# Kernel optimization log

Measured on AMD Instinct MI355X. Metric: run time of the kernel, lower is better.

## Reference

```python
import jax, jax.numpy as jnp
import numpy as np

EPS = 1e-6
KH, KW = 3, 3
SH, SW = 1, 1


def _unfold(x, kh, kw, sh, sw):
    # x: [N, C, H, W] -> patches [N, C, kh*kw, L], L = ox*oy (torch.nn.Unfold layout)
    N, C, H, W = x.shape
    ox = (H - kh) // sh + 1
    oy = (W - kw) // sw + 1
    pats = [x[:, :, i:i + sh * ox:sh, j:j + sw * oy:sw]
            for i in range(kh) for j in range(kw)]
    p = jnp.stack(pats, axis=2)  # [N, C, K, ox, oy]
    return p.reshape(N, C, kh * kw, ox * oy), ox, oy


def setup_inputs() -> dict:
    key = jax.random.key(0)
    kx, k1, k2 = jax.random.split(key, 3)
    x = jax.random.uniform(kx, (32, 2, 64, 64, 64), dtype=jnp.float32)
    w1 = jax.random.uniform(k1, (64, KH * KW), dtype=jnp.float32)
    w2 = jax.random.uniform(k2, (128, 64), dtype=jnp.float32)
    return {"x": x, "w1": w1, "w2": w2}


def reference(x, w1, w2):
    B = x.shape[0]
    out_ch = w2.shape[0]
    xr = x[:, 0]  # rotation plane [B, C, H, W]
    xa = x[:, 1]  # magnitude plane

    pr, ox, oy = _unfold(xr, KH, KW, SH, SW)  # [B, C, K, L]
    pa, _, _ = _unfold(xa, KH, KW, SH, SW)

    # weightNormalize1: squared weights normalized by GLOBAL sum (rot branch)
    w1_glob = w1 ** 2 / jnp.sum(w1 ** 2)
    w2_glob = w2 ** 2 / jnp.sum(w2 ** 2)
    # weightNormalize (drop_prob=0): squared weights normalized PER ROW (abs branch)
    w1_row = w1 ** 2 / jnp.sum(w1 ** 2, axis=1, keepdims=True)
    w2_row = w2 ** 2 / jnp.sum(w2 ** 2, axis=1, keepdims=True)

    # rotation branch: two weighted contractions
    rot = jnp.einsum('bckl,ck->bcl', pr, w1_glob)          # [B, C, L]
    out_rot = jnp.einsum('bcl,oc->bol', rot, w2_glob)      # [B, O, L]
    out_rot = out_rot.reshape(B, 1, out_ch, ox, oy)

    # magnitude branch: log -> weighted contractions -> exp
    la = jnp.log(pa + EPS)                                  # [B, C, K, L]
    a1 = jnp.einsum('bckl,ck->bcl', la, w1_row)             # [B, C, L]
    out_abs = jnp.exp(jnp.einsum('bcl,oc->bol', a1, w2_row))
    out_abs = out_abs.reshape(B, 1, out_ch, ox, oy)

    return jnp.concatenate([out_rot, out_abs], axis=1)  # [B, 2, O, ox, oy]
```

## Files before the change

### kernel.cpp

```cpp
#include <hip/hip_runtime.h>
#include <cstdint>
#include <cstddef>

#define EPSF 1e-6f

typedef __attribute__((ext_vector_type(4))) float f32x4;
typedef __attribute__((ext_vector_type(8))) short s16x8;

static __device__ __forceinline__ unsigned short f2bf(float f) {
    unsigned u = __float_as_uint(f);
    u += 0x7FFFu + ((u >> 16) & 1u);
    return (unsigned short)(u >> 16);
}
static __device__ __forceinline__ float bf2f(unsigned short h) {
    return __uint_as_float(((unsigned)h) << 16);
}
static __device__ __forceinline__ unsigned packHL(float v) {
    unsigned short h = f2bf(v);
    float r = v - bf2f(h);
    unsigned short l = f2bf(r);
    return ((unsigned)h << 16) | (unsigned)l;
}

__global__ __launch_bounds__(256) void prep_weights(const float* __restrict__ w1,
                                                    const float* __restrict__ w2,
                                                    float* __restrict__ ws) {
    __shared__ float part1[4], part2[4];
    __shared__ float s1row[64];
    __shared__ float s2row[128];
    __shared__ float tot[2];

    const int t = threadIdx.x;
    const int ln = t & 63;
    const int wv = t >> 6;

    float s1 = 0.f;
    for (int i = t; i < 64 * 9; i += 256) { float v = w1[i]; s1 += v * v; }
    float s2 = 0.f;
    const float4* w2v = (const float4*)w2;
    for (int i = t; i < 2048; i += 256) {
        float4 v = w2v[i];
        s2 += v.x * v.x + v.y * v.y + v.z * v.z + v.w * v.w;
    }
    #pragma unroll
    for (int d = 32; d > 0; d >>= 1) {
        s1 += __shfl_down(s1, d);
        s2 += __shfl_down(s2, d);
    }
    if (ln == 0) { part1[wv] = s1; part2[wv] = s2; }

    if (t < 64) {
        float rs = 0.f;
        #pragma unroll
        for (int k = 0; k < 9; ++k) { float v = w1[t * 9 + k]; rs += v * v; }
        s1row[t] = rs;
    } else if (t < 192) {
        const int o = t - 64;
        float rs = 0.f;
        const float4* p = (const float4*)(w2 + o * 64);
        #pragma unroll
        for (int k = 0; k < 16; ++k) {
            float4 v = p[k];
            rs += v.x * v.x + v.y * v.y + v.z * v.z + v.w * v.w;
        }
        s2row[o] = rs;
    }
    __syncthreads();
    if (t == 0) tot[0] = part1[0] + part1[1] + part1[2] + part1[3];
    if (t == 1) tot[1] = part2[0] + part2[1] + part2[2] + part2[3];
    __syncthreads();

    const float t1 = tot[0];
    const float t2 = tot[1];
    for (int i = t; i < 64 * 9; i += 256) {
        float q = w1[i] * w1[i];
        ws[i] = q / t1;
        ws[576 + i] = q / s1row[i / 9];
    }
    unsigned* wsu = (unsigned*)ws;
    for (int i = t; i < 8192; i += 256) {
        float q = w2[i] * w2[i];
        wsu[1152 + i]        = packHL(q / t2);
        wsu[1152 + 8192 + i] = packHL(q / s2row[i >> 6]);
    }
}

__global__ __launch_bounds__(256) void conv_fused(const float* __restrict__ x,
                                                  const float* __restrict__ ws,
                                                  float* __restrict__ out) {
    const int h = blockIdx.x;
    const int branch = blockIdx.y;
    const int b = blockIdx.z;
    const int t = threadIdx.x;
    const int lane = t & 63;
    const int wv = __builtin_amdgcn_readfirstlane(t >> 6);
    const int lm = lane & 15;
    const int quad = lane >> 4;

    __shared__ unsigned rotT[64 * 65];

    const float* __restrict__ w1n = ws + branch * 576;
    const unsigned* __restrict__ w2p = (const unsigned*)ws + 1152 + branch * 8192;
    const float* __restrict__ xb = x + (size_t)(b * 2 + branch) * (64 * 4096);

    #pragma unroll 4
    for (int i = 0; i < 16; ++i) {
        const int c = wv * 16 + i;
        const float* xp = xb + c * 4096 + h * 64 + lane;
        float r0 = xp[0];
        float r1 = xp[64];
        float r2 = xp[128];
        if (branch) {
            r0 = __logf(r0 + EPSF);
            r1 = __logf(r1 + EPSF);
            r2 = __logf(r2 + EPSF);
        }
        const float* wc = w1n + c * 9;
        const float a1 = __shfl_down(r0, 1), a2 = __shfl_down(r0, 2);
        const float b1 = __shfl_down(r1, 1), b2 = __shfl_down(r1, 2);
        const float c1 = __shfl_down(r2, 1), c2 = __shfl_down(r2, 2);
        float s = r0 * wc[0] + a1 * wc[1] + a2 * wc[2]
                + r1 * wc[3] + b1 * wc[4] + b2 * wc[5]
                + r2 * wc[6] + c1 * wc[7] + c2 * wc[8];
        rotT[lane * 65 + c] = packHL(s);
    }
    __syncthreads();

    s16x8 aH[2][2], aL[2][2];
    #pragma unroll
    for (int mt = 0; mt < 2; ++mt) {
        #pragma unroll
        for (int kk = 0; kk < 2; ++kk) {
            const unsigned* p = w2p + (wv * 32 + mt * 16 + lm) * 64 + kk * 32 + quad * 8;
            #pragma unroll
            for (int j = 0; j < 8; ++j) {
                unsigned u = p[j];
                aH[mt][kk][j] = (short)(u >> 16);
                aL[mt][kk][j] = (short)(u & 0xffffu);
            }
        }
    }

    f32x4 acc[2][4];
    #pragma unroll
    for (int mt = 0; mt < 2; ++mt)
        #pragma unroll
        for (int nt = 0; nt < 4; ++nt)
            acc[mt][nt] = (f32x4){0.f, 0.f, 0.f, 0.f};

    #pragma unroll
    for (int nt = 0; nt < 4; ++nt) {
        #pragma unroll
        for (int kk = 0; kk < 2; ++kk) {
            const unsigned* lp = &rotT[(nt * 16 + lm) * 65 + kk * 32 + quad * 8];
            s16x8 bH, bL;
            #pragma unroll
            for (int j = 0; j < 8; ++j) {
                unsigned u = lp[j];
                bH[j] = (short)(u >> 16);
                bL[j] = (short)(u & 0xffffu);
            }
            #pragma unroll
            for (int mt = 0; mt < 2; ++mt) {
                acc[mt][nt] = __builtin_amdgcn_mfma_f32_16x16x32_bf16(aH[mt][kk], bH, acc[mt][nt], 0, 0, 0);
                acc[mt][nt] = __builtin_amdgcn_mfma_f32_16x16x32_bf16(aH[mt][kk], bL, acc[mt][nt], 0, 0, 0);
                acc[mt][nt] = __builtin_amdgcn_mfma_f32_16x16x32_bf16(aL[mt][kk], bH, acc[mt][nt], 0, 0, 0);
            }
        }
    }

    #pragma unroll
    for (int mt = 0; mt < 2; ++mt) {
        const int oc0 = wv * 32 + mt * 16 + quad * 4;
        #pragma unroll
        for (int nt = 0; nt < 4; ++nt) {
            const int px = nt * 16 + lm;
            if (px < 62) {
                const size_t base =
                    ((size_t)((b * 2 + branch) * 128 + oc0)) * 3844 + (size_t)h * 62 + px;
                #pragma unroll
                for (int r = 0; r < 4; ++r) {
                    float v = acc[mt][nt][r];
                    if (branch) v = __expf(v);
                    out[base + (size_t)r * 3844] = v;
                }
            }
        }
    }
}

extern "C" void kernel_launch(void* const* d_in, const int* in_sizes, int n_in,
                              void* d_out, int out_size, void* d_ws, size_t ws_size,
                              hipStream_t stream) {
    const float* x  = (const float*)d_in[0];
    const float* w1 = (const float*)d_in[1];
    const float* w2 = (const float*)d_in[2];
    float* out = (float*)d_out;
    float* ws  = (float*)d_ws;

    prep_weights<<<1, 256, 0, stream>>>(w1, w2, ws);

    dim3 grid(62, 2, 32);
    conv_fused<<<grid, 256, 0, stream>>>(x, ws, out);
}
```

Measured before the change: 238.6 us.

## Vectorize depthwise stage with float4 loads and perm-based bf16 split

Result: faster. 219.1 us (-8.1%).

```diff
diff --git a/kernel.cpp b/kernel.cpp
--- a/kernel.cpp
+++ b/kernel.cpp
@@ -6,6 +6,7 @@
 
 typedef __attribute__((ext_vector_type(4))) float f32x4;
 typedef __attribute__((ext_vector_type(8))) short s16x8;
+typedef union { s16x8 v; unsigned u[4]; } s16x8u;
 
 static __device__ __forceinline__ unsigned short f2bf(float f) {
     unsigned u = __float_as_uint(f);
@@ -73,9 +74,12 @@
     const float t1 = tot[0];
     const float t2 = tot[1];
     for (int i = t; i < 64 * 9; i += 256) {
+        const int c = i / 9;
+        const int k = i - c * 9;
+        const int idx = (c >> 4) * 144 + (c & 3) * 36 + ((c >> 2) & 3) * 9 + k;
         float q = w1[i] * w1[i];
-        ws[i] = q / t1;
-        ws[576 + i] = q / s1row[i / 9];
+        ws[idx] = q / t1;
+        ws[576 + idx] = q / s1row[c];
     }
     unsigned* wsu = (unsigned*)ws;
     for (int i = t; i < 8192; i += 256) {
@@ -96,50 +100,80 @@
     const int wv = __builtin_amdgcn_readfirstlane(t >> 6);
     const int lm = lane & 15;
     const int quad = lane >> 4;
+    const int c4 = lm;
+    const int chsub = quad;
 
     __shared__ unsigned rotT[64 * 65];
 
-    const float* __restrict__ w1n = ws + branch * 576;
+    const float* __restrict__ w1t = ws + branch * 576;
     const unsigned* __restrict__ w2p = (const unsigned*)ws + 1152 + branch * 8192;
     const float* __restrict__ xb = x + (size_t)(b * 2 + branch) * (64 * 4096);
 
-    #pragma unroll 4
-    for (int i = 0; i < 16; ++i) {
-        const int c = wv * 16 + i;
-        const float* xp = xb + c * 4096 + h * 64 + lane;
-        float r0 = xp[0];
-        float r1 = xp[64];
-        float r2 = xp[128];
+    const float* xrow = xb + h * 64 + 4 * c4;
+    #pragma unroll 2
+    for (int cg = 0; cg < 4; ++cg) {
+        const int c = wv * 16 + cg * 4 + chsub;
+        const float* xp = xrow + c * 4096;
+        float4 v0 = *(const float4*)xp;
+        float4 v1 = *(const float4*)(xp + 64);
+        float4 v2 = *(const float4*)(xp + 128);
         if (branch) {
-            r0 = __logf(r0 + EPSF);
-            r1 = __logf(r1 + EPSF);
-            r2 = __logf(r2 + EPSF);
-        }
-        const float* wc = w1n + c * 9;
-        const float a1 = __shfl_down(r0, 1), a2 = __shfl_down(r0, 2);
-        const float b1 = __shfl_down(r1, 1), b2 = __shfl_down(r1, 2);
-        const float c1 = __shfl_down(r2, 1), c2 = __shfl_down(r2, 2);
-        float s = r0 * wc[0] + a1 * wc[1] + a2 * wc[2]
-                + r1 * wc[3] + b1 * wc[4] + b2 * wc[5]
-                + r2 * wc[6] + c1 * wc[7] + c2 * wc[8];
-        rotT[lane * 65 + c] = packHL(s);
-    }
-    __syncthreads();
-
-    s16x8 aH[2][2], aL[2][2];
+            v0.x = __logf(v0.x + EPSF); v0.y = __logf(v0.y + EPSF);
+            v0.z = __logf(v0.z + EPSF); v0.w = __logf(v0.w + EPSF);
+            v1.x = __logf(v1.x + EPSF); v1.y = __logf(v1.y + EPSF);
+            v1.z = __logf(v1.z + EPSF); v1.w = __logf(v1.w + EPSF);
+            v2.x = __logf(v2.x + EPSF); v2.y = __logf(v2.y + EPSF);
+            v2.z = __logf(v2.z + EPSF); v2.w = __logf(v2.w + EPSF);
+        }
+        const float sx0 = __shfl_down(v0.x, 1), sy0 = __shfl_down(v0.y, 1);
+        const float sx1 = __shfl_down(v1.x, 1), sy1 = __shfl_down(v1.y, 1);
+        const float sx2 = __shfl_down(v2.x, 1), sy2 = __shfl_down(v2.y, 1);
+        const float* wc = w1t + wv * 144 + chsub * 36 + cg * 9;
+        const float w0 = wc[0], w1_ = wc[1], w2_ = wc[2];
+        const float w3 = wc[3], w4 = wc[4], w5 = wc[5];
+        const float w6 = wc[6], w7 = wc[7], w8 = wc[8];
+        float p0 = v0.x * w0 + v0.y * w1_ + v0.z * w2_
+                 + v1.x * w3 + v1.y * w4  + v1.z * w5
+                 + v2.x * w6 + v2.y * w7  + v2.z * w8;
+        float p1 = v0.y * w0 + v0.z * w1_ + v0.w * w2_
+                 + v1.y * w3 + v1.z * w4  + v1.w * w5
+                 + v2.y * w6 + v2.z * w7  + v2.w * w8;
+        float p2 = v0.z * w0 + v0.w * w1_ + sx0 * w2_
+                 + v1.z * w3 + v1.w * w4  + sx1 * w5
+                 + v2.z * w6 + v2.w * w7  + sx2 * w8;
+        float p3 = v0.w * w0 + sx0 * w1_ + sy0 * w2_
+                 + v1.w * w3 + sx1 * w4  + sy1 * w5
+                 + v2.w * w6 + sx2 * w7  + sy2 * w8;
+        unsigned* rp = &rotT[(4 * c4) * 65 + c];
+        rp[0]   = packHL(p0);
+        rp[65]  = packHL(p1);
+        rp[130] = packHL(p2);
+        rp[195] = packHL(p3);
+    }
+
+    unsigned araw[2][2][8];
     #pragma unroll
     for (int mt = 0; mt < 2; ++mt) {
         #pragma unroll
         for (int kk = 0; kk < 2; ++kk) {
             const unsigned* p = w2p + (wv * 32 + mt * 16 + lm) * 64 + kk * 32 + quad * 8;
             #pragma unroll
-            for (int j = 0; j < 8; ++j) {
-                unsigned u = p[j];
-                aH[mt][kk][j] = (short)(u >> 16);
-                aL[mt][kk][j] = (short)(u & 0xffffu);
-            }
-        }
-    }
+            for (int j = 0; j < 8; ++j) araw[mt][kk][j] = p[j];
+        }
+    }
+    __syncthreads();
+
+    s16x8u aH[2][2], aL[2][2];
+    #pragma unroll
+    for (int mt = 0; mt < 2; ++mt)
+        #pragma unroll
+        for (int kk = 0; kk < 2; ++kk)
+            #pragma unroll
+            for (int j2 = 0; j2 < 4; ++j2) {
+                unsigned u0 = araw[mt][kk][2 * j2], u1 = araw[mt][kk][2 * j2 + 1];
+                aH[mt][kk].u[j2] = __builtin_amdgcn_perm(u1, u0, 0x07060302u);
+                aL[mt][kk].u[j2] = __builtin_amdgcn_perm(u1, u0, 0x05040100u);
+            }
 
     f32x4 acc[2][4];
     #pragma unroll
@@ -153,18 +187,18 @@
         #pragma unroll
         for (int kk = 0; kk < 2; ++kk) {
             const unsigned* lp = &rotT[(nt * 16 + lm) * 65 + kk * 32 + quad * 8];
-            s16x8 bH, bL;
-            #pragma unroll
-            for (int j = 0; j < 8; ++j) {
-                unsigned u = lp[j];
-                bH[j] = (short)(u >> 16);
-                bL[j] = (short)(u & 0xffffu);
+            s16x8u bH, bL;
+            #pragma unroll
+            for (int j2 = 0; j2 < 4; ++j2) {
+                unsigned u0 = lp[2 * j2], u1 = lp[2 * j2 + 1];
+                bH.u[j2] = __builtin_amdgcn_perm(u1, u0, 0x07060302u);
+                bL.u[j2] = __builtin_amdgcn_perm(u1, u0, 0x05040100u);
             }
             #pragma unroll
             for (int mt = 0; mt < 2; ++mt) {
-                acc[mt][nt] = __builtin_amdgcn_mfma_f32_16x16x32_bf16(aH[mt][kk], bH, acc[mt][nt], 0, 0, 0);
-                acc[mt][nt] = __builtin_amdgcn_mfma_f32_16x16x32_bf16(aH[mt][kk], bL, acc[mt][nt], 0, 0, 0);
-                acc[mt][nt] = __builtin_amdgcn_mfma_f32_16x16x32_bf16(aL[mt][kk], bH, acc[mt][nt], 0, 0, 0);
+                acc[mt][nt] = __builtin_amdgcn_mfma_f32_16x16x32_bf16(aH[mt][kk].v, bH.v, acc[mt][nt], 0, 0, 0);
+                acc[mt][nt] = __builtin_amdgcn_mfma_f32_16x16x32_bf16(aH[mt][kk].v, bL.v, acc[mt][nt], 0, 0, 0);
+                acc[mt][nt] = __builtin_amdgcn_mfma_f32_16x16x32_bf16(aL[mt][kk].v, bH.v, acc[mt][nt], 0, 0, 0);
             }
         }
     }
```
